# Kernel optimization log

Measured on AMD Instinct MI355X. Metric: run time of the kernel, lower is better.

## Reference

```python
import jax, jax.numpy as jnp
import numpy as np

B, F, E = 4096, 39, 16
FIELD_DIMS = [1000] * F
OFFSETS = jnp.asarray(np.concatenate([[0], np.cumsum(FIELD_DIMS)[:-1]]).astype(np.int64))
I_IDX, J_IDX = np.triu_indices(F, 1)  # 741 pairs (i<j)
I_IDX = jnp.asarray(I_IDX); J_IDX = jnp.asarray(J_IDX)
MLP_DIMS = [2 * 741 * E, 400, 400, 400]
EPS = 1e-5


def setup_inputs() -> dict:
    key = jax.random.key(0)
    ks = jax.random.split(key, 20)
    s = 0.02
    inp = {
        'x': jax.random.randint(ks[0], (B, F), 0, 1000, dtype=jnp.int64),
        'emb': jax.random.normal(ks[1], (sum(FIELD_DIMS), E), jnp.float32) * s,
        'sen_w1': jax.random.normal(ks[2], (F, F), jnp.float32) * s,
        'sen_b1': jnp.zeros((F,), jnp.float32),
        'sen_w2': jax.random.normal(ks[3], (F, F), jnp.float32) * s,
        'sen_b2': jnp.zeros((F,), jnp.float32),
        'Wb1': jax.random.normal(ks[4], (E, E), jnp.float32) * s,
        'Wb2': jax.random.normal(ks[5], (E, E), jnp.float32) * s,
    }
    for li in range(3):
        din, dout = MLP_DIMS[li], MLP_DIMS[li + 1]
        inp[f'mw{li}'] = jax.random.normal(ks[6 + li], (dout, din), jnp.float32) * s
        inp[f'mb{li}'] = jnp.zeros((dout,), jnp.float32)
        inp[f'g{li}'] = jnp.ones((dout,), jnp.float32)
        inp[f'be{li}'] = jnp.zeros((dout,), jnp.float32)
    inp['mw3'] = jax.random.normal(ks[9], (1, MLP_DIMS[-1]), jnp.float32) * s
    inp['mb3'] = jnp.zeros((1,), jnp.float32)
    return inp


def _bilinear_all(v, W):
    # v: [B,F,E]; p_ij = (v_i W^T) * v_j for all i<j -> [B, P*E]
    proj = jnp.einsum('bfe,de->bfd', v, W)
    p = proj[:, I_IDX] * v[:, J_IDX]  # [B, 741, E]
    return p.reshape(v.shape[0], -1)


def _bn(h, g, be):
    mu = h.mean(axis=0)
    var = h.var(axis=0)
    return g * (h - mu) * jax.lax.rsqrt(var + EPS) + be


def _forward(x, emb, sen_w1, sen_b1, sen_w2, sen_b2, Wb1, Wb2,
             mw0, mb0, g0, be0, mw1, mb1, g1, be1, mw2, mb2, g2, be2, mw3, mb3):
    xe = emb[x + OFFSETS[None, :]]  # [B,F,E]
    # SENet: max over embed dim, two-layer excitation with ReLU
    z = jnp.max(xe, axis=2)  # [B,F]
    a = jax.nn.relu(jax.nn.relu(z @ sen_w1.T + sen_b1) @ sen_w2.T + sen_b2)  # [B,F]
    x_sen = a[:, :, None] * xe
    x_con = jnp.concatenate([_bilinear_all(xe, Wb1), _bilinear_all(x_sen, Wb2)], axis=1)
    h = x_con
    for w, b, g, be in ((mw0, mb0, g0, be0), (mw1, mb1, g1, be1), (mw2, mb2, g2, be2)):
        h = jax.nn.relu(_bn(h @ w.T + b, g, be))  # dropout = identity (eval)
    return h @ mw3.T + mb3  # [B,1]


def reference(x, emb, sen_w1, sen_b1, sen_w2, sen_b2, Wb1, Wb2,
              mw0, mb0, g0, be0, mw1, mb1, g1, be1, mw2, mb2, g2, be2, mw3, mb3):
    return _forward(x, emb, sen_w1, sen_b1, sen_w2, sen_b2, Wb1, Wb2,
                    mw0, mb0, g0, be0, mw1, mb1, g1, be1, mw2, mb2, g2, be2, mw3, mb3)
```

## Files before the change

### kernel.cpp

```cpp
#include <hip/hip_runtime.h>
#include <stdint.h>

#define B_ROWS  4096
#define F_FIELDS 39
#define NPAIR   741
#define XCON_K  23712
#define KP      23744
#define NP      512
#define HID     400
#define SPLITK0 8
#define KITERS0 (KP/64)

#define OFF_XCON 0ull
#define SZ_XCON  ((size_t)B_ROWS * KP * 2)
#define OFF_W0B  (OFF_XCON + SZ_XCON)
#define SZ_W0B   ((size_t)NP * KP * 2)
#define OFF_W1B  (OFF_W0B + SZ_W0B)
#define SZ_WSM   ((size_t)NP * NP * 2)
#define OFF_W2B  (OFF_W1B + SZ_WSM)
#define OFF_HPRE (OFF_W2B + SZ_WSM)
#define SZ_HPRE  ((size_t)B_ROWS * NP * 4)
#define OFF_HN   (OFF_HPRE + SZ_HPRE)
#define SZ_HN    ((size_t)B_ROWS * NP * 2)
#define OFF_STATS (OFF_HN + SZ_HN)
#define SZ_STATS  (6 * 512 * 4)
#define WS_NEEDED (OFF_STATS + SZ_STATS + 4096)

__device__ __forceinline__ unsigned short f2bf(float f) {
    union { float f; unsigned u; } v; v.f = f;
    unsigned r = (v.u + 0x7FFFu + ((v.u >> 16) & 1u)) >> 16;
    return (unsigned short)r;
}
__device__ __forceinline__ float bf2f(unsigned short h) {
    union { unsigned u; float f; } v; v.u = ((unsigned)h) << 16;
    return v.f;
}
__device__ __forceinline__ void gl_lds16(const void* g, void* l) {
    __builtin_amdgcn_global_load_lds(
        (const __attribute__((address_space(1))) void*)g,
        (__attribute__((address_space(3))) void*)l, 16, 0, 0);
}

typedef __bf16 bf16x8 __attribute__((ext_vector_type(8)));
typedef float  floatx4 __attribute__((ext_vector_type(4)));

__global__ __launch_bounds__(256) void build_all(
    const int* __restrict__ x, const float* __restrict__ emb,
    const float* __restrict__ w1, const float* __restrict__ b1,
    const float* __restrict__ w2, const float* __restrict__ b2,
    const float* __restrict__ Wb1, const float* __restrict__ Wb2,
    unsigned short* __restrict__ xcon,
    const float* __restrict__ mw0, unsigned short* __restrict__ w0b,
    const float* __restrict__ mw1, const float* __restrict__ mw2,
    unsigned short* __restrict__ w1b, unsigned short* __restrict__ w2b)
{
    __shared__ float xe[624], p0[624], sp[624], sx[624];
    __shared__ float zz[40], tt[40], aa[40];
    __shared__ short itab[NPAIR], jtab[NPAIR];
    const int bb = blockIdx.x, tid = threadIdx.x;

    if (bb >= B_ROWS) {
        if (bb < B_ROWS + NP) {
            const int o = bb - B_ROWS;
            for (int k4 = tid; k4 < KP / 4; k4 += 256) {
                const int k = k4 * 4;
                unsigned short u[4] = {0, 0, 0, 0};
                if (o < HID && k < XCON_K) {
                    float4 v = *(const float4*)&mw0[(size_t)o * XCON_K + k];
                    u[0] = f2bf(v.x); u[1] = f2bf(v.y); u[2] = f2bf(v.z); u[3] = f2bf(v.w);
                }
                uint2 pk; pk.x = u[0] | ((unsigned)u[1] << 16); pk.y = u[2] | ((unsigned)u[3] << 16);
                *(uint2*)&w0b[(size_t)o * KP + k] = pk;
            }
        } else {
            const int idx = bb - B_ROWS - NP;
            const int which = idx >> 9;
            const int o = idx & 511;
            const float* w = which ? mw2 : mw1;
            unsigned short* o_ = which ? w2b : w1b;
            for (int k = tid; k < NP; k += 256) {
                float v = (o < HID && k < HID) ? w[o * HID + k] : 0.f;
                o_[o * NP + k] = f2bf(v);
            }
        }
        return;
    }

    const int b = bb;
    for (int p = tid; p < NPAIR; p += 256) {
        float fp = (float)p;
        int i = (int)(38.5f - sqrtf(38.5f * 38.5f - 2.f * fp));
        while (i > 0 && p < (i * (77 - i)) / 2) --i;
        while (p >= ((i + 1) * (76 - i)) / 2) ++i;
        itab[p] = (short)i;
        jtab[p] = (short)(i + 1 + (p - (i * (77 - i)) / 2));
    }
    if (tid < 156) {
        int f = tid >> 2, e4 = (tid & 3) * 4;
        int row = x[b * F_FIELDS + f] + 1000 * f;
        *(float4*)&xe[f * 16 + e4] = *(const float4*)&emb[row * 16 + e4];
    }
    __syncthreads();
    if (tid < F_FIELDS) {
        float m = xe[tid * 16];
        for (int e = 1; e < 16; ++e) m = fmaxf(m, xe[tid * 16 + e]);
        zz[tid] = m;
    }
    __syncthreads();
    if (tid < F_FIELDS) {
        float s = b1[tid];
        for (int g = 0; g < F_FIELDS; ++g) s += zz[g] * w1[tid * F_FIELDS + g];
        tt[tid] = fmaxf(s, 0.f);
    }
    __syncthreads();
    if (tid < F_FIELDS) {
        float s = b2[tid];
        for (int g = 0; g < F_FIELDS; ++g) s += tt[g] * w2[tid * F_FIELDS + g];
        aa[tid] = fmaxf(s, 0.f);
    }
    __syncthreads();
    for (int idx = tid; idx < 624; idx += 256) {
        int f = idx >> 4, d = idx & 15;
        float s1 = 0.f, s2 = 0.f;
        for (int e = 0; e < 16; ++e) {
            float v = xe[f * 16 + e];
            s1 += v * Wb1[d * 16 + e];
            s2 += v * Wb2[d * 16 + e];
        }
        const float af = aa[f];
        p0[idx] = s1;
        sp[idx] = af * s2;
        sx[idx] = af * xe[idx];
    }
    __syncthreads();
    uint4* out4 = (uint4*)(xcon + (size_t)b * KP);
    for (int s = tid; s < 2968; s += 256) {
        uint4 w;
        if (s < 2964) {
            const int p2 = s >> 1;
            const int hi = s & 1;
            const int half = (p2 >= NPAIR);
            const int p = p2 - NPAIR * half;
            const int i = itab[p], j = jtab[p];
            const float* pr = (half ? &sp[i * 16] : &p0[i * 16]) + hi * 8;
            const float* xr = (half ? &sx[j * 16] : &xe[j * 16]) + hi * 8;
            unsigned short u[8];
#pragma unroll
            for (int q = 0; q < 2; ++q) {
                float4 a = *(const float4*)(pr + q * 4);
                float4 bx = *(const float4*)(xr + q * 4);
                u[q * 4 + 0] = f2bf(a.x * bx.x);
                u[q * 4 + 1] = f2bf(a.y * bx.y);
                u[q * 4 + 2] = f2bf(a.z * bx.z);
                u[q * 4 + 3] = f2bf(a.w * bx.w);
            }
            w.x = u[0] | ((unsigned)u[1] << 16);
            w.y = u[2] | ((unsigned)u[3] << 16);
            w.z = u[4] | ((unsigned)u[5] << 16);
            w.w = u[6] | ((unsigned)u[7] << 16);
        } else {
            w.x = w.y = w.z = w.w = 0u;
        }
        out4[s] = w;
    }
}

__global__ __launch_bounds__(256, 4) void gemm0(
    const unsigned short* __restrict__ A, const unsigned short* __restrict__ Bm,
    float* __restrict__ C, int kcnt)
{
    __shared__ __align__(16) unsigned short As[128 * 64];
    __shared__ __align__(16) unsigned short Bs[128 * 64];
    const int tid = threadIdx.x;
    const int m0 = blockIdx.y * 128, n0 = blockIdx.x * 128;
    int kb = blockIdx.z * kcnt;
    int ke = kb + kcnt; if (ke > KITERS0) ke = KITERS0;

    const int swz = (((tid & 7) ^ ((tid >> 3) & 7)) * 8);
    const unsigned short* Ag = A + (size_t)(m0 + (tid >> 3)) * KP + swz;
    const unsigned short* Bg = Bm + (size_t)(n0 + (tid >> 3)) * KP + swz;
    unsigned short* Asl = As + tid * 8;
    unsigned short* Bsl = Bs + tid * 8;

    const int wv = tid >> 6, ln = tid & 63;
    const int wm = (wv >> 1) * 64, wn = (wv & 1) * 64;
    const int l15 = ln & 15, lq = ln >> 4;
    const int xorm = l15 & 7;

    floatx4 acc[4][4];
#pragma unroll
    for (int mi = 0; mi < 4; ++mi)
#pragma unroll
        for (int ni = 0; ni < 4; ++ni)
            acc[mi][ni] = (floatx4){0.f, 0.f, 0.f, 0.f};

    for (int kt = kb; kt < ke; ++kt) {
        const size_t ko = (size_t)kt * 64;
#pragma unroll
        for (int i = 0; i < 4; ++i)
            gl_lds16(Ag + (size_t)(i * 32) * KP + ko, Asl + i * 2048);
#pragma unroll
        for (int i = 0; i < 4; ++i)
            gl_lds16(Bg + (size_t)(i * 32) * KP + ko, Bsl + i * 2048);
        __syncthreads();
#pragma unroll
        for (int kk = 0; kk < 64; kk += 32) {
            bf16x8 af[4], bfr[4];
#pragma unroll
            for (int t = 0; t < 4; ++t) {
                af[t]  = *(const bf16x8*)(As + (wm + t * 16 + l15) * 64
                                             + ((((kk >> 3) + lq) ^ xorm) * 8));
                bfr[t] = *(const bf16x8*)(Bs + (wn + t * 16 + l15) * 64
                                             + ((((kk >> 3) + lq) ^ xorm) * 8));
            }
#pragma unroll
            for (int mi = 0; mi < 4; ++mi)
#pragma unroll
                for (int ni = 0; ni < 4; ++ni)
                    acc[mi][ni] = __builtin_amdgcn_mfma_f32_16x16x32_bf16(
                        af[mi], bfr[ni], acc[mi][ni], 0, 0, 0);
        }
        __syncthreads();
    }
#pragma unroll
    for (int mi = 0; mi < 4; ++mi)
#pragma unroll
        for (int ni = 0; ni < 4; ++ni) {
            const int col = n0 + wn + ni * 16 + l15;
            const int row0 = m0 + wm + mi * 16 + lq * 4;
#pragma unroll
            for (int r = 0; r < 4; ++r)
                atomicAdd(&C[(size_t)(row0 + r) * NP + col], acc[mi][ni][r]);
        }
}

__global__ __launch_bounds__(256) void colstats(const float* __restrict__ H,
                                                float* __restrict__ cs, float* __restrict__ csq) {
    const int tid = threadIdx.x;
    const int c4 = (tid & 127) * 4;
    const int ro = tid >> 7;
    const int r0 = blockIdx.x * 16;
    float s0 = 0, s1 = 0, s2 = 0, s3 = 0, q0 = 0, q1 = 0, q2 = 0, q3 = 0;
#pragma unroll
    for (int i = 0; i < 8; ++i) {
        float4 v = *(const float4*)&H[(size_t)(r0 + ro + 2 * i) * NP + c4];
        s0 += v.x; q0 += v.x * v.x;  s1 += v.y; q1 += v.y * v.y;
        s2 += v.z; q2 += v.z * v.z;  s3 += v.w; q3 += v.w * v.w;
    }
    atomicAdd(&cs[c4], s0); atomicAdd(&cs[c4 + 1], s1);
    atomicAdd(&cs[c4 + 2], s2); atomicAdd(&cs[c4 + 3], s3);
    atomicAdd(&csq[c4], q0); atomicAdd(&csq[c4 + 1], q1);
    atomicAdd(&csq[c4 + 2], q2); atomicAdd(&csq[c4 + 3], q3);
}

template<int MODE>
__global__ __launch_bounds__(256) void gemm_bn(
    const void* __restrict__ Ain, const unsigned short* __restrict__ Bm,
    const float* __restrict__ cs, const float* __restrict__ csq,
    const float* __restrict__ g, const float* __restrict__ be,
    void* __restrict__ Cout, float* __restrict__ csO, float* __restrict__ csqO)
{
    __shared__ __align__(16) unsigned short As[64 * 64];
    __shared__ __align__(16) unsigned short Bs[64 * 64];
    __shared__ float sc[NP], sh[NP];
    const int tid = threadIdx.x;
    const int m0 = blockIdx.y * 64, n0 = blockIdx.x * 64;

    for (int c = tid; c < NP; c += 256) {
        float mean = cs[c] * (1.f / 4096.f);
        float var  = csq[c] * (1.f / 4096.f) - mean * mean;
        float s = (c < HID ? g[c] : 0.f) * rsqrtf(var + 1e-5f);
        sc[c] = s;
        sh[c] = (c < HID ? be[c] : 0.f) - mean * s;
    }

    const int r = tid >> 3, c8 = tid & 7;
    const int gsw = c8 ^ (r & 7);
    const unsigned short* Bg = Bm + (size_t)(n0 + r) * NP + gsw * 8;
    unsigned short* Bsl = Bs + tid * 8;

    const int wv = tid >> 6, ln = tid & 63;
    const int wm = (wv >> 1) * 32, wn = (wv & 1) * 32;
    const int l15 = ln & 15, lq = ln >> 4;
    const int xorm = l15 & 7;

    floatx4 acc[2][2];
#pragma unroll
    for (int mi = 0; mi < 2; ++mi)
#pragma unroll
        for (int ni = 0; ni < 2; ++ni)
            acc[mi][ni] = (floatx4){0.f, 0.f, 0.f, 0.f};

    __syncthreads();

    for (int kt = 0; kt < NP / 64; ++kt) {
        const int ko = kt * 64;
        const int kc = ko + gsw * 8;
#pragma unroll
        for (int i = 0; i < 2; ++i) {
            const int row = m0 + r + i * 32;
            unsigned short u[8];
            if (MODE == 0) {
                const float* ap = (const float*)Ain + (size_t)row * NP + kc;
                float4 v0 = *(const float4*)ap;
                float4 v1 = *(const float4*)(ap + 4);
                u[0] = f2bf(fmaxf(v0.x * sc[kc]     + sh[kc],     0.f));
                u[1] = f2bf(fmaxf(v0.y * sc[kc + 1] + sh[kc + 1], 0.f));
                u[2] = f2bf(fmaxf(v0.z * sc[kc + 2] + sh[kc + 2], 0.f));
                u[3] = f2bf(fmaxf(v0.w * sc[kc + 3] + sh[kc + 3], 0.f));
                u[4] = f2bf(fmaxf(v1.x * sc[kc + 4] + sh[kc + 4], 0.f));
                u[5] = f2bf(fmaxf(v1.y * sc[kc + 5] + sh[kc + 5], 0.f));
                u[6] = f2bf(fmaxf(v1.z * sc[kc + 6] + sh[kc + 6], 0.f));
                u[7] = f2bf(fmaxf(v1.w * sc[kc + 7] + sh[kc + 7], 0.f));
            } else {
                const unsigned short* ap = (const unsigned short*)Ain + (size_t)row * NP + kc;
                uint4 pk = *(const uint4*)ap;
                unsigned short raw[8] = {
                    (unsigned short)(pk.x & 0xFFFF), (unsigned short)(pk.x >> 16),
                    (unsigned short)(pk.y & 0xFFFF), (unsigned short)(pk.y >> 16),
                    (unsigned short)(pk.z & 0xFFFF), (unsigned short)(pk.z >> 16),
                    (unsigned short)(pk.w & 0xFFFF), (unsigned short)(pk.w >> 16)};
#pragma unroll
                for (int e = 0; e < 8; ++e)
                    u[e] = f2bf(fmaxf(bf2f(raw[e]) * sc[kc + e] + sh[kc + e], 0.f));
            }
            uint4 w;
            w.x = u[0] | ((unsigned)u[1] << 16);
            w.y = u[2] | ((unsigned)u[3] << 16);
            w.z = u[4] | ((unsigned)u[5] << 16);
            w.w = u[6] | ((unsigned)u[7] << 16);
            *(uint4*)(As + (r + i * 32) * 64 + c8 * 8) = w;
        }
#pragma unroll
        for (int i = 0; i < 2; ++i)
            gl_lds16(Bg + (size_t)(i * 32) * NP + ko, Bsl + i * 2048);
        __syncthreads();
#pragma unroll
        for (int kk = 0; kk < 64; kk += 32) {
            bf16x8 af[2], bfr[2];
#pragma unroll
            for (int t = 0; t < 2; ++t) {
                af[t]  = *(const bf16x8*)(As + (wm + t * 16 + l15) * 64
                                             + ((((kk >> 3) + lq) ^ xorm) * 8));
                bfr[t] = *(const bf16x8*)(Bs + (wn + t * 16 + l15) * 64
                                             + ((((kk >> 3) + lq) ^ xorm) * 8));
            }
#pragma unroll
            for (int mi = 0; mi < 2; ++mi)
#pragma unroll
                for (int ni = 0; ni < 2; ++ni)
                    acc[mi][ni] = __builtin_amdgcn_mfma_f32_16x16x32_bf16(
                        af[mi], bfr[ni], acc[mi][ni], 0, 0, 0);
        }
        __syncthreads();
    }
#pragma unroll
    for (int mi = 0; mi < 2; ++mi)
#pragma unroll
        for (int ni = 0; ni < 2; ++ni) {
            const int col = n0 + wn + ni * 16 + l15;
            const int row0 = m0 + wm + mi * 16 + lq * 4;
#pragma unroll
            for (int rr = 0; rr < 4; ++rr) {
                if (MODE == 0)
                    ((unsigned short*)Cout)[(size_t)(row0 + rr) * NP + col] = f2bf(acc[mi][ni][rr]);
                else
                    ((float*)Cout)[(size_t)(row0 + rr) * NP + col] = acc[mi][ni][rr];
            }
        }
#pragma unroll
    for (int ni = 0; ni < 2; ++ni) {
        float s = 0.f, q = 0.f;
#pragma unroll
        for (int mi = 0; mi < 2; ++mi)
#pragma unroll
            for (int rr = 0; rr < 4; ++rr) { float v = acc[mi][ni][rr]; s += v; q += v * v; }
        s += __shfl_down(s, 32); q += __shfl_down(q, 32);
        s += __shfl_down(s, 16); q += __shfl_down(q, 16);
        if (lq == 0) {
            const int col = n0 + wn + ni * 16 + l15;
            atomicAdd(&csO[col], s);
            atomicAdd(&csqO[col], q);
        }
    }
}

__global__ __launch_bounds__(256) void bnrelu_dot(const float* __restrict__ H,
                       const float* __restrict__ cs, const float* __restrict__ csq,
                       const float* __restrict__ g, const float* __restrict__ be,
                       const float* __restrict__ w3, const float* __restrict__ b3,
                       float* __restrict__ out) {
    __shared__ float sc[NP], sh[NP], ww[NP];
    for (int c = threadIdx.x; c < NP; c += 256) {
        float mean = cs[c] * (1.f / 4096.f);
        float var  = csq[c] * (1.f / 4096.f) - mean * mean;
        float s = (c < HID ? g[c] : 0.f) * rsqrtf(var + 1e-5f);
        sc[c] = s;
        sh[c] = (c < HID ? be[c] : 0.f) - mean * s;
        ww[c] = (c < HID ? w3[c] : 0.f);
    }
    __syncthreads();
    const int wv = threadIdx.x >> 6, ln = threadIdx.x & 63;
    const int row = blockIdx.x * 4 + wv;
    const float4* hp = (const float4*)(H + (size_t)row * NP);
    float s = 0.f;
#pragma unroll
    for (int it = 0; it < 2; ++it) {
        const int c4 = it * 64 + ln;
        const int c = c4 * 4;
        float4 v = hp[c4];
        s += fmaxf(v.x * sc[c]     + sh[c],     0.f) * ww[c]
           + fmaxf(v.y * sc[c + 1] + sh[c + 1], 0.f) * ww[c + 1]
           + fmaxf(v.z * sc[c + 2] + sh[c + 2], 0.f) * ww[c + 2]
           + fmaxf(v.w * sc[c + 3] + sh[c + 3], 0.f) * ww[c + 3];
    }
#pragma unroll
    for (int o = 32; o; o >>= 1) s += __shfl_down(s, o);
    if (ln == 0) out[row] = s + b3[0];
}

extern "C" void kernel_launch(void* const* d_in, const int* in_sizes, int n_in,
                              void* d_out, int out_size, void* d_ws, size_t ws_size,
                              hipStream_t stream)
{
    const int*   x    = (const int*)d_in[0];
    const float* emb  = (const float*)d_in[1];
    const float* sw1  = (const float*)d_in[2];
    const float* sb1  = (const float*)d_in[3];
    const float* sw2  = (const float*)d_in[4];
    const float* sb2  = (const float*)d_in[5];
    const float* Wb1  = (const float*)d_in[6];
    const float* Wb2  = (const float*)d_in[7];
    const float* mw0  = (const float*)d_in[8];
    const float* g0   = (const float*)d_in[10];
    const float* be0  = (const float*)d_in[11];
    const float* mw1  = (const float*)d_in[12];
    const float* g1   = (const float*)d_in[14];
    const float* be1  = (const float*)d_in[15];
    const float* mw2  = (const float*)d_in[16];
    const float* g2   = (const float*)d_in[18];
    const float* be2  = (const float*)d_in[19];
    const float* mw3  = (const float*)d_in[20];
    const float* mb3  = (const float*)d_in[21];
    (void)in_sizes; (void)n_in; (void)out_size;
    if (ws_size < WS_NEEDED) return;

    char* ws = (char*)d_ws;
    unsigned short* xcon = (unsigned short*)(ws + OFF_XCON);
    unsigned short* w0b  = (unsigned short*)(ws + OFF_W0B);
    unsigned short* w1b  = (unsigned short*)(ws + OFF_W1B);
    unsigned short* w2b  = (unsigned short*)(ws + OFF_W2B);
    float* hpre = (float*)(ws + OFF_HPRE);
    unsigned short* hn = (unsigned short*)(ws + OFF_HN);
    float* stats = (float*)(ws + OFF_STATS);
    float* cs0 = stats,        *csq0 = stats + 512;
    float* cs1 = stats + 1024, *csq1 = stats + 1536;
    float* cs2 = stats + 2048, *csq2 = stats + 2560;

    build_all<<<B_ROWS + NP + 2 * NP, 256, 0, stream>>>(
        x, emb, sw1, sb1, sw2, sb2, Wb1, Wb2, xcon, mw0, w0b, mw1, mw2, w1b, w2b);

    hipMemsetAsync(hpre, 0, SZ_HPRE, stream);
    hipMemsetAsync(stats, 0, SZ_STATS, stream);

    gemm0<<<dim3(NP / 128, B_ROWS / 128, SPLITK0), 256, 0, stream>>>(
        xcon, w0b, hpre, (KITERS0 + SPLITK0 - 1) / SPLITK0);
    colstats<<<256, 256, 0, stream>>>(hpre, cs0, csq0);

    gemm_bn<0><<<dim3(NP / 64, B_ROWS / 64), 256, 0, stream>>>(
        hpre, w1b, cs0, csq0, g0, be0, hn, cs1, csq1);

    gemm_bn<1><<<dim3(NP / 64, B_ROWS / 64), 256, 0, stream>>>(
        hn, w2b, cs1, csq1, g1, be1, hpre, cs2, csq2);

    bnrelu_dot<<<B_ROWS / 4, 256, 0, stream>>>(hpre, cs2, csq2, g2, be2, mw3, mb3, (float*)d_out);
}
```

Before: 424.1 us.

## Fold hpre/stats zeroing into build kernel, widen xcon writes, remap gemm0 blocks

Replaces the two memset launches with 17 extra blocks in build_all that zero the stats buffer and the split-K accumulator hpre. Each build thread now writes one full 16-element pair (two uint4 stores) instead of half a pair. gemm0 also remaps its linear block index so the split-K slices of the same output tile are scheduled next to each other, which may improve cache reuse and reduce atomic contention. The goal is fewer launches and better locality, at the cost of more register use per thread in the build phase.

Measured after the change: 401.0 us. 5.4% less time.

```diff
diff --git a/kernel.cpp b/kernel.cpp
--- a/kernel.cpp
+++ b/kernel.cpp
@@ -26,6 +26,8 @@
 #define SZ_STATS  (6 * 512 * 4)
 #define WS_NEEDED (OFF_STATS + SZ_STATS + 4096)
 
+#define ZBLK 17
+
 __device__ __forceinline__ unsigned short f2bf(float f) {
     union { float f; unsigned u; } v; v.f = f;
     unsigned r = (v.u + 0x7FFFu + ((v.u >> 16) & 1u)) >> 16;
@@ -52,7 +54,8 @@
     unsigned short* __restrict__ xcon,
     const float* __restrict__ mw0, unsigned short* __restrict__ w0b,
     const float* __restrict__ mw1, const float* __restrict__ mw2,
-    unsigned short* __restrict__ w1b, unsigned short* __restrict__ w2b)
+    unsigned short* __restrict__ w1b, unsigned short* __restrict__ w2b,
+    float* __restrict__ hpre, float* __restrict__ stats)
 {
     __shared__ float xe[624], p0[624], sp[624], sx[624];
     __shared__ float zz[40], tt[40], aa[40];
@@ -72,7 +75,7 @@
                 uint2 pk; pk.x = u[0] | ((unsigned)u[1] << 16); pk.y = u[2] | ((unsigned)u[3] << 16);
                 *(uint2*)&w0b[(size_t)o * KP + k] = pk;
             }
-        } else {
+        } else if (bb < B_ROWS + NP + 2 * NP) {
             const int idx = bb - B_ROWS - NP;
             const int which = idx >> 9;
             const int o = idx & 511;
@@ -82,6 +85,15 @@
                 float v = (o < HID && k < HID) ? w[o * HID + k] : 0.f;
                 o_[o * NP + k] = f2bf(v);
             }
+        } else {
+            const int zi = bb - (B_ROWS + NP + 2 * NP);
+            if (zi == 0) {
+                for (int i = tid; i < 6 * 512; i += 256) stats[i] = 0.f;
+            } else {
+                float4* p = (float4*)hpre + (size_t)(zi - 1) * 32768;
+                float4 z4; z4.x = z4.y = z4.z = z4.w = 0.f;
+                for (int i = tid; i < 32768; i += 256) p[i] = z4;
+            }
         }
         return;
     }
@@ -133,20 +145,17 @@
         sx[idx] = af * xe[idx];
     }
     __syncthreads();
-    uint4* out4 = (uint4*)(xcon + (size_t)b * KP);
-    for (int s = tid; s < 2968; s += 256) {
-        uint4 w;
-        if (s < 2964) {
-            const int p2 = s >> 1;
-            const int hi = s & 1;
-            const int half = (p2 >= NPAIR);
-            const int p = p2 - NPAIR * half;
+    unsigned short* out = xcon + (size_t)b * KP;
+    for (int c = tid; c < 1484; c += 256) {
+        if (c < 2 * NPAIR) {
+            const int half = (c >= NPAIR);
+            const int p = c - NPAIR * half;
             const int i = itab[p], j = jtab[p];
-            const float* pr = (half ? &sp[i * 16] : &p0[i * 16]) + hi * 8;
-            const float* xr = (half ? &sx[j * 16] : &xe[j * 16]) + hi * 8;
-            unsigned short u[8];
-#pragma unroll
-            for (int q = 0; q < 2; ++q) {
+            const float* pr = half ? &sp[i * 16] : &p0[i * 16];
+            const float* xr = half ? &sx[j * 16] : &xe[j * 16];
+            unsigned short u[16];
+#pragma unroll
+            for (int q = 0; q < 4; ++q) {
                 float4 a = *(const float4*)(pr + q * 4);
                 float4 bx = *(const float4*)(xr + q * 4);
                 u[q * 4 + 0] = f2bf(a.x * bx.x);
@@ -154,14 +163,17 @@
                 u[q * 4 + 2] = f2bf(a.z * bx.z);
                 u[q * 4 + 3] = f2bf(a.w * bx.w);
             }
-            w.x = u[0] | ((unsigned)u[1] << 16);
-            w.y = u[2] | ((unsigned)u[3] << 16);
-            w.z = u[4] | ((unsigned)u[5] << 16);
-            w.w = u[6] | ((unsigned)u[7] << 16);
+            uint4 v0, v1;
+            v0.x = u[0] | ((unsigned)u[1] << 16);  v0.y = u[2] | ((unsigned)u[3] << 16);
+            v0.z = u[4] | ((unsigned)u[5] << 16);  v0.w = u[6] | ((unsigned)u[7] << 16);
+            v1.x = u[8] | ((unsigned)u[9] << 16);  v1.y = u[10] | ((unsigned)u[11] << 16);
+            v1.z = u[12] | ((unsigned)u[13] << 16); v1.w = u[14] | ((unsigned)u[15] << 16);
+            uint4* dst = (uint4*)(out + (half ? 11856 : 0) + p * 16);
+            dst[0] = v0; dst[1] = v1;
         } else {
-            w.x = w.y = w.z = w.w = 0u;
-        }
-        out4[s] = w;
+            uint4 z4; z4.x = z4.y = z4.z = z4.w = 0u;
+            ((uint4*)(out + XCON_K))[c - 2 * NPAIR] = z4;
+        }
     }
 }
 
@@ -172,8 +184,13 @@
     __shared__ __align__(16) unsigned short As[128 * 64];
     __shared__ __align__(16) unsigned short Bs[128 * 64];
     const int tid = threadIdx.x;
-    const int m0 = blockIdx.y * 128, n0 = blockIdx.x * 128;
-    int kb = blockIdx.z * kcnt;
+    const int l = blockIdx.x + 4 * blockIdx.y + 128 * blockIdx.z;
+    const int zI = l & 7;
+    const int s  = l >> 3;
+    const int nI = s & 3;
+    const int mI = s >> 2;
+    const int m0 = mI * 128, n0 = nI * 128;
+    int kb = zI * kcnt;
     int ke = kb + kcnt; if (ke > KITERS0) ke = KITERS0;
 
     const int swz = (((tid & 7) ^ ((tid >> 3) & 7)) * 8);
@@ -457,11 +474,9 @@
     float* cs1 = stats + 1024, *csq1 = stats + 1536;
     float* cs2 = stats + 2048, *csq2 = stats + 2560;
 
-    build_all<<<B_ROWS + NP + 2 * NP, 256, 0, stream>>>(
-        x, emb, sw1, sb1, sw2, sb2, Wb1, Wb2, xcon, mw0, w0b, mw1, mw2, w1b, w2b);
-
-    hipMemsetAsync(hpre, 0, SZ_HPRE, stream);
-    hipMemsetAsync(stats, 0, SZ_STATS, stream);
+    build_all<<<B_ROWS + NP + 2 * NP + ZBLK, 256, 0, stream>>>(
+        x, emb, sw1, sb1, sw2, sb2, Wb1, Wb2, xcon, mw0, w0b, mw1, mw2, w1b, w2b,
+        hpre, stats);
 
     gemm0<<<dim3(NP / 128, B_ROWS / 128, SPLITK0), 256, 0, stream>>>(
         xcon, w0b, hpre, (KITERS0 + SPLITK0 - 1) / SPLITK0);
```
